# Optimization experiments

Measured on AMD Instinct MI355X. Metric: run time of the kernel, lower is better.

The kernel has to match this reference:

```python
import jax, jax.numpy as jnp
import numpy as np

B, S, D, H, DK, DFF = 4, 1024, 1024, 16, 64, 4096
EPS = 1e-5


def layer_norm(x, g, b):
    m = jnp.mean(x, axis=-1, keepdims=True)
    v = jnp.var(x, axis=-1, keepdims=True)
    return (x - m) * jax.lax.rsqrt(v + EPS) * g + b


def setup_inputs() -> dict:
    key = jax.random.key(0)
    ks = jax.random.split(key, 12)
    sc = 0.02
    return {
        "x":    jax.random.normal(ks[0], (B, S, D), jnp.float32),
        # per-head Q/K/V projections, stacked over heads: [H, D, DK]
        "Wq":   jax.random.normal(ks[1], (H, D, DK), jnp.float32) * sc,
        "bq":   jnp.zeros((H, DK), jnp.float32),
        "Wk":   jax.random.normal(ks[2], (H, D, DK), jnp.float32) * sc,
        "bk":   jnp.zeros((H, DK), jnp.float32),
        "Wv":   jax.random.normal(ks[3], (H, D, DK), jnp.float32) * sc,
        "bv":   jnp.zeros((H, DK), jnp.float32),
        # output projection: [H*DK, D]
        "Wo":   jax.random.normal(ks[4], (H * DK, D), jnp.float32) * sc,
        "bo":   jnp.zeros((D,), jnp.float32),
        # FFN
        "W1":   jax.random.normal(ks[5], (D, DFF), jnp.float32) * sc,
        "b1":   jnp.zeros((DFF,), jnp.float32),
        "W2":   jax.random.normal(ks[6], (DFF, D), jnp.float32) * sc,
        "b2":   jnp.zeros((D,), jnp.float32),
        # LayerNorms
        "g1":   jnp.ones((D,), jnp.float32),
        "be1":  jnp.zeros((D,), jnp.float32),
        "g2":   jnp.ones((D,), jnp.float32),
        "be2":  jnp.zeros((D,), jnp.float32),
    }


def reference(x, Wq, bq, Wk, bk, Wv, bv, Wo, bo, W1, b1, W2, b2, g1, be1, g2, be2):
    # batched multi-head attention (original loops per head; math identical)
    q = jnp.einsum("bsd,hdk->bhsk", x, Wq) + bq[None, :, None, :]
    k = jnp.einsum("bsd,hdk->bhsk", x, Wk) + bk[None, :, None, :]
    v = jnp.einsum("bsd,hdk->bhsk", x, Wv) + bv[None, :, None, :]
    scale = 1.0 / jnp.sqrt(jnp.asarray(DK, x.dtype))
    scores = jnp.einsum("bhsk,bhtk->bhst", q * scale, k)
    attn = jax.nn.softmax(scores, axis=-1)  # dropout = eval-mode identity
    o = jnp.einsum("bhst,bhtk->bhsk", attn, v)
    # torch.cat over heads along dim 2 -> [B, S, H*DK]
    o = jnp.transpose(o, (0, 2, 1, 3)).reshape(B, S, H * DK)
    att = o @ Wo + bo
    # post-attn: residual of LayerNorm(att)
    x = x + layer_norm(att, g1, be1)
    # FFN
    pos = jax.nn.relu(x @ W1 + b1) @ W2 + b2
    x = x + layer_norm(pos, g2, be2)
    return x
```

## Files before the change

kernel.cpp:

```cpp
#include <hip/hip_runtime.h>
#include <hip/hip_bf16.h>

typedef unsigned short u16;
typedef short bf16x8_t __attribute__((ext_vector_type(8)));
typedef float f32x4_t  __attribute__((ext_vector_type(4)));

__device__ __forceinline__ u16 f2bf(float f) {
    __hip_bfloat16 h = __float2bfloat16(f);
    union { __hip_bfloat16 b; u16 u; } cv; cv.b = h; return cv.u;
}

__device__ __forceinline__ void g2l16(const void* g, void* l) {
    __builtin_amdgcn_global_load_lds(
        (const __attribute__((address_space(1))) unsigned int*)g,
        (__attribute__((address_space(3))) unsigned int*)l, 16, 0, 0);
}

__global__ __launch_bounds__(256) void k_cast_bf16v(const float* __restrict__ in,
                                                    u16* __restrict__ out, int n4) {
    int i = blockIdx.x * 256 + threadIdx.x;
    if (i < n4) {
        float4 f = ((const float4*)in)[i];
        ushort4 o;
        o.x = f2bf(f.x); o.y = f2bf(f.y); o.z = f2bf(f.z); o.w = f2bf(f.w);
        ((ushort4*)out)[i] = o;
    }
}

__global__ __launch_bounds__(256)
void k_transpose3(const float* __restrict__ Wo, const float* __restrict__ W1,
                  const float* __restrict__ W2, u16* __restrict__ Wot,
                  u16* __restrict__ W1t, u16* __restrict__ W2t) {
    int id = blockIdx.x;
    const float* in; u16* out; int R, C, tx, ty;
    if (id < 256)       { in = Wo; out = Wot; R = 1024; C = 1024; tx = id & 15; ty = id >> 4; }
    else if (id < 1280) { id -= 256; in = W1; out = W1t; R = 1024; C = 4096; tx = id & 63; ty = id >> 6; }
    else                { id -= 1280; in = W2; out = W2t; R = 4096; C = 1024; tx = id & 15; ty = id >> 4; }
    __shared__ float t[64][65];
    int r0 = ty * 64, c0 = tx * 64;
    int lc = threadIdx.x & 63, lr = threadIdx.x >> 6;
#pragma unroll
    for (int p = 0; p < 16; ++p) {
        int rr = p * 4 + lr;
        t[rr][lc] = in[(size_t)(r0 + rr) * C + c0 + lc];
    }
    __syncthreads();
#pragma unroll
    for (int p = 0; p < 16; ++p) {
        int cc = p * 4 + lr;
        out[(size_t)(c0 + cc) * R + r0 + lc] = f2bf(t[lc][cc]);
    }
}

__global__ __launch_bounds__(256)
void k_qkvw_t(const float* __restrict__ Wq, const float* __restrict__ Wk,
              const float* __restrict__ Wv, u16* __restrict__ out) {
    const float* in = blockIdx.z == 0 ? Wq : (blockIdx.z == 1 ? Wk : Wv);
    in += (size_t)blockIdx.y * 65536;
    u16* o = out + ((size_t)blockIdx.z * 1024 + blockIdx.y * 64) * 1024;
    __shared__ float t[64][65];
    int d0 = blockIdx.x * 64;
    int lc = threadIdx.x & 63, lr = threadIdx.x >> 6;
#pragma unroll
    for (int p = 0; p < 16; ++p) {
        int rr = p * 4 + lr;
        t[rr][lc] = in[(size_t)(d0 + rr) * 64 + lc];
    }
    __syncthreads();
#pragma unroll
    for (int p = 0; p < 16; ++p) {
        int cc = p * 4 + lr;
        o[(size_t)cc * 1024 + d0 + lc] = f2bf(t[lc][cc]);
    }
}

__global__ __launch_bounds__(256)
void k_vt(const u16* __restrict__ V, u16* __restrict__ VT) {
    __shared__ u16 t[64 * 72];
    int bh = blockIdx.y, s0 = blockIdx.x * 64;
    const u16* Vp = V + (size_t)bh * 65536;
    u16* Tp = VT + (size_t)bh * 65536;
    int tid = threadIdx.x;
    int r = tid >> 3, c = (tid & 7) * 8;
    *(uint4*)&t[r * 72 + c]        = *(const uint4*)&Vp[(size_t)(s0 + r) * 64 + c];
    *(uint4*)&t[(r + 32) * 72 + c] = *(const uint4*)&Vp[(size_t)(s0 + r + 32) * 64 + c];
    __syncthreads();
    int d = tid >> 2, sl0 = (tid & 3) * 16;
    uint4 outv[2];
    u16* ov = (u16*)outv;
#pragma unroll
    for (int j = 0; j < 16; ++j) ov[j] = t[(sl0 + j) * 72 + d];
    *(uint4*)&Tp[(size_t)d * 1024 + s0 + sl0]     = outv[0];
    *(uint4*)&Tp[(size_t)d * 1024 + s0 + sl0 + 8] = outv[1];
}

template<int EPI>
__global__ __launch_bounds__(256)
void k_gemm_bt(const u16* __restrict__ A, const u16* __restrict__ Bt,
               const float* __restrict__ bias0, void* __restrict__ out,
               int M, int N, int K, int kchunk)
{
    __shared__ __align__(16) u16 As[2 * 128 * 32];
    __shared__ __align__(16) u16 Bs[2 * 128 * 32];
    int tid = threadIdx.x;
    int wave = tid >> 6, lane = tid & 63;
    int row0 = blockIdx.y * 128, col0 = blockIdx.x * 128;
    int z = blockIdx.z;
    int kbeg = z * kchunk;

    int lrow = lane >> 2, lcol = (lane & 3) * 8;
    const u16* pA0 = A  + (size_t)(row0 + wave * 16 + lrow) * K + kbeg + lcol;
    const u16* pA1 = pA0 + (size_t)64 * K;
    const u16* pB0 = Bt + (size_t)(col0 + wave * 16 + lrow) * K + kbeg + lcol;
    const u16* pB1 = pB0 + (size_t)64 * K;
    u16* lA0 = &As[wave * 512];
    u16* lA1 = &As[2048 + wave * 512];
    u16* lB0 = &Bs[wave * 512];
    u16* lB1 = &Bs[2048 + wave * 512];

    int wm = (wave >> 1) * 64, wn = (wave & 1) * 64;
    int quad = lane >> 4, l16 = lane & 15;

    f32x4_t acc[4][4];
#pragma unroll
    for (int i = 0; i < 4; i++)
#pragma unroll
        for (int j = 0; j < 4; j++) acc[i][j] = f32x4_t{0.f, 0.f, 0.f, 0.f};

    for (int kk = 0; kk < kchunk; kk += 64) {
        __syncthreads();
        g2l16(pA0, lA0);      g2l16(pA1, lA1);
        g2l16(pA0 + 32, lA0 + 4096); g2l16(pA1 + 32, lA1 + 4096);
        g2l16(pB0, lB0);      g2l16(pB1, lB1);
        g2l16(pB0 + 32, lB0 + 4096); g2l16(pB1 + 32, lB1 + 4096);
        pA0 += 64; pA1 += 64; pB0 += 64; pB1 += 64;
        __syncthreads();

#pragma unroll
        for (int s = 0; s < 2; ++s) {
            const u16* as = &As[s * 4096];
            const u16* bs = &Bs[s * 4096];
            bf16x8_t a[4], b[4];
#pragma unroll
            for (int i = 0; i < 4; ++i)
                a[i] = *(const bf16x8_t*)&as[(wm + i * 16 + l16) * 32 + quad * 8];
#pragma unroll
            for (int j = 0; j < 4; ++j)
                b[j] = *(const bf16x8_t*)&bs[(wn + j * 16 + l16) * 32 + quad * 8];
#pragma unroll
            for (int i = 0; i < 4; ++i)
#pragma unroll
                for (int j = 0; j < 4; ++j)
                    acc[i][j] = __builtin_amdgcn_mfma_f32_16x16x32_bf16(a[i], b[j], acc[i][j], 0, 0, 0);
        }
    }

#pragma unroll
    for (int i = 0; i < 4; ++i)
#pragma unroll
        for (int j = 0; j < 4; ++j)
#pragma unroll
            for (int r = 0; r < 4; ++r) {
                int row = row0 + wm + i * 16 + quad * 4 + r;
                int col = col0 + wn + j * 16 + l16;
                ((float*)out)[(size_t)z * M * N + (size_t)row * N + col] = acc[i][j][r];
            }
}

template<int EPI>
__global__ __launch_bounds__(512, 4)
void k_gemm_bt2(const u16* __restrict__ A, const u16* __restrict__ Bt,
                const float* __restrict__ bias0, const float* __restrict__ bias1,
                const float* __restrict__ bias2, void* __restrict__ out,
                int M, int N, int K)
{
    __shared__ __align__(16) u16 As[2 * 256 * 32];
    __shared__ __align__(16) u16 Bs[2 * 128 * 32];
    int tid = threadIdx.x;
    int wave = tid >> 6, lane = tid & 63;
    int row0 = blockIdx.y * 256, col0 = blockIdx.x * 128;

    int lrow = lane >> 2, lcol = (lane & 3) * 8;
    const u16* pA0 = A  + (size_t)(row0 + wave * 16 + lrow) * K + lcol;
    const u16* pA1 = pA0 + (size_t)128 * K;
    const u16* pB0 = Bt + (size_t)(col0 + wave * 16 + lrow) * K + lcol;
    u16* lA0 = &As[wave * 512];
    u16* lA1 = &As[4096 + wave * 512];
    u16* lB0 = &Bs[wave * 512];

    int wm = (wave >> 1) * 64, wn = (wave & 1) * 64;
    int quad = lane >> 4, l16 = lane & 15;

    f32x4_t acc[4][4];
#pragma unroll
    for (int i = 0; i < 4; i++)
#pragma unroll
        for (int j = 0; j < 4; j++) acc[i][j] = f32x4_t{0.f, 0.f, 0.f, 0.f};

    for (int kk = 0; kk < K; kk += 64) {
        __syncthreads();
        g2l16(pA0, lA0);           g2l16(pA1, lA1);
        g2l16(pA0 + 32, lA0 + 8192); g2l16(pA1 + 32, lA1 + 8192);
        g2l16(pB0, lB0);           g2l16(pB0 + 32, lB0 + 4096);
        pA0 += 64; pA1 += 64; pB0 += 64;
        __syncthreads();

#pragma unroll
        for (int s = 0; s < 2; ++s) {
            const u16* as = &As[s * 8192];
            const u16* bs = &Bs[s * 4096];
            bf16x8_t a[4], b[4];
#pragma unroll
            for (int i = 0; i < 4; ++i)
                a[i] = *(const bf16x8_t*)&as[(wm + i * 16 + l16) * 32 + quad * 8];
#pragma unroll
            for (int j = 0; j < 4; ++j)
                b[j] = *(const bf16x8_t*)&bs[(wn + j * 16 + l16) * 32 + quad * 8];
#pragma unroll
            for (int i = 0; i < 4; ++i)
#pragma unroll
                for (int j = 0; j < 4; ++j)
                    acc[i][j] = __builtin_amdgcn_mfma_f32_16x16x32_bf16(a[i], b[j], acc[i][j], 0, 0, 0);
        }
    }

#pragma unroll
    for (int i = 0; i < 4; ++i)
#pragma unroll
        for (int j = 0; j < 4; ++j)
#pragma unroll
            for (int r = 0; r < 4; ++r) {
                int row = row0 + wm + i * 16 + quad * 4 + r;
                int col = col0 + wn + j * 16 + l16;
                float v = acc[i][j][r];
                if (EPI == 1) {
                    ((u16*)out)[(size_t)row * N + col] = f2bf(fmaxf(v + bias0[col], 0.f));
                } else {
                    int proj = col >> 10, within = col & 1023;
                    const float* bp = proj == 0 ? bias0 : (proj == 1 ? bias1 : bias2);
                    v += bp[within];
                    if (proj == 0) v *= 0.18033688f;
                    int h = within >> 6, kq = within & 63;
                    int b_ = row >> 10, s_ = row & 1023;
                    size_t bh = (size_t)((b_ << 4) + h);
                    ((u16*)out)[(size_t)proj * 4194304 + bh * 65536 + (s_ << 6) + kq] = f2bf(v);
                }
            }
}

__global__ __launch_bounds__(512, 4)
void k_attn(const u16* __restrict__ Qg, const u16* __restrict__ Kg,
            const u16* __restrict__ VTg, u16* __restrict__ Og)
{
    __shared__ __align__(16) u16 Ks[64 * 64];
    __shared__ __align__(16) u16 Vs[64 * 64];
    __shared__ __align__(16) u16 Ps[128 * 64];

    int tid = threadIdx.x, wave = tid >> 6, lane = tid & 63;
    int quad = lane >> 4, l16 = lane & 15;
    int bh = blockIdx.y;
    int q0 = blockIdx.x * 128;
    int wrow = wave * 16;

    const u16* Qp  = Qg  + (size_t)bh * 65536;
    const u16* Kp  = Kg  + (size_t)bh * 65536;
    const u16* VTp = VTg + (size_t)bh * 65536;

    int arow_g = q0 + wrow + l16;
    bf16x8_t aq0 = *(const bf16x8_t*)&Qp[(size_t)arow_g * 64 + quad * 8];
    bf16x8_t aq1 = *(const bf16x8_t*)&Qp[(size_t)arow_g * 64 + 32 + quad * 8];

    int srow = tid >> 3, scb = tid & 7;
    uint4 kreg = *(const uint4*)&Kp[(size_t)srow * 64 + scb * 8];
    uint4 vreg = *(const uint4*)&VTp[(size_t)srow * 1024 + scb * 8];
    u16* kdst = &Ks[srow * 64 + ((scb ^ (srow & 7)) * 8)];
    u16* vdst = &Vs[srow * 64 + ((scb ^ (srow & 7)) * 8)];

    f32x4_t o[4], lsum;
#pragma unroll
    for (int nt = 0; nt < 4; ++nt) o[nt] = f32x4_t{0.f, 0.f, 0.f, 0.f};
    lsum = f32x4_t{0.f, 0.f, 0.f, 0.f};

    bf16x8_t ones;
#pragma unroll
    for (int j = 0; j < 8; ++j) ones[j] = (short)0x3F80;

    int a7 = l16 & 7;

    for (int kv0 = 0; kv0 < 1024; kv0 += 64) {
        __syncthreads();
        *(uint4*)kdst = kreg;
        *(uint4*)vdst = vreg;
        __syncthreads();
        if (kv0 < 960) {
            kreg = *(const uint4*)&Kp[(size_t)(kv0 + 64 + srow) * 64 + scb * 8];
            vreg = *(const uint4*)&VTp[(size_t)srow * 1024 + kv0 + 64 + scb * 8];
        }

        f32x4_t s[4];
#pragma unroll
        for (int nt = 0; nt < 4; ++nt) {
            int brow = nt * 16 + l16;
            bf16x8_t bk0 = *(const bf16x8_t*)&Ks[brow * 64 + ((quad ^ a7) * 8)];
            bf16x8_t bk1 = *(const bf16x8_t*)&Ks[brow * 64 + (((4 + quad) ^ a7) * 8)];
            s[nt] = __builtin_amdgcn_mfma_f32_16x16x32_bf16(aq0, bk0, f32x4_t{0.f,0.f,0.f,0.f}, 0, 0, 0);
            s[nt] = __builtin_amdgcn_mfma_f32_16x16x32_bf16(aq1, bk1, s[nt], 0, 0, 0);
        }

#pragma unroll
        for (int nt = 0; nt < 4; ++nt) {
            int pcb = nt * 2 + (l16 >> 3);
#pragma unroll
            for (int r = 0; r < 4; ++r) {
                float p = exp2f(s[nt][r]);
                int pr = wrow + quad * 4 + r;
                Ps[pr * 64 + ((pcb ^ (pr & 7)) * 8) + (l16 & 7)] = f2bf(p);
            }
        }

        int arow = wrow + l16;
        bf16x8_t ap0 = *(const bf16x8_t*)&Ps[arow * 64 + ((quad ^ a7) * 8)];
        bf16x8_t ap1 = *(const bf16x8_t*)&Ps[arow * 64 + (((4 + quad) ^ a7) * 8)];
#pragma unroll
        for (int nt = 0; nt < 4; ++nt) {
            int vrow = nt * 16 + l16;
            bf16x8_t bv0 = *(const bf16x8_t*)&Vs[vrow * 64 + ((quad ^ a7) * 8)];
            bf16x8_t bv1 = *(const bf16x8_t*)&Vs[vrow * 64 + (((4 + quad) ^ a7) * 8)];
            o[nt] = __builtin_amdgcn_mfma_f32_16x16x32_bf16(ap0, bv0, o[nt], 0, 0, 0);
            o[nt] = __builtin_amdgcn_mfma_f32_16x16x32_bf16(ap1, bv1, o[nt], 0, 0, 0);
        }
        lsum = __builtin_amdgcn_mfma_f32_16x16x32_bf16(ap0, ones, lsum, 0, 0, 0);
        lsum = __builtin_amdgcn_mfma_f32_16x16x32_bf16(ap1, ones, lsum, 0, 0, 0);
    }

    int b = bh >> 4, h = bh & 15;
    float invl[4];
#pragma unroll
    for (int r = 0; r < 4; ++r) invl[r] = 1.f / lsum[r];
#pragma unroll
    for (int nt = 0; nt < 4; ++nt)
#pragma unroll
        for (int r = 0; r < 4; ++r) {
            int srow2 = q0 + wrow + quad * 4 + r;
            Og[(size_t)(b * 1024 + srow2) * 1024 + (h << 6) + nt * 16 + l16] = f2bf(o[nt][r] * invl[r]);
        }
}

template<int MODE>
__global__ __launch_bounds__(256)
void k_ln2(const float* __restrict__ p0, const float* __restrict__ p1,
           const float* __restrict__ bias, const float* __restrict__ residf,
           const u16* __restrict__ residb, const float* __restrict__ g,
           const float* __restrict__ be, float* __restrict__ out,
           u16* __restrict__ outb)
{
    int row = blockIdx.x, tid = threadIdx.x;
    size_t base = (size_t)row * 1024;
    float xv[4]; float s = 0.f, sq = 0.f;
#pragma unroll
    for (int i = 0; i < 4; i++) {
        int c = tid + i * 256;
        xv[i] = p0[base + c] + p1[base + c] + bias[c];
        s += xv[i]; sq += xv[i] * xv[i];
    }
#pragma unroll
    for (int off = 32; off; off >>= 1) { s += __shfl_down(s, off); sq += __shfl_down(sq, off); }
    __shared__ float ss[4], ssq[4];
    int wv = tid >> 6;
    if ((tid & 63) == 0) { ss[wv] = s; ssq[wv] = sq; }
    __syncthreads();
    s  = ss[0] + ss[1] + ss[2] + ss[3];
    sq = ssq[0] + ssq[1] + ssq[2] + ssq[3];
    float mean = s * (1.f / 1024.f);
    float var  = sq * (1.f / 1024.f) - mean * mean;
    float rstd = rsqrtf(var + 1e-5f);
#pragma unroll
    for (int i = 0; i < 4; i++) {
        int c = tid + i * 256;
        float rv;
        if (MODE == 0) rv = residf[base + c];
        else {
            union { u16 u[2]; unsigned int w; float f; } cv;
            cv.w = (unsigned int)residb[base + c] << 16;
            rv = cv.f;
        }
        float y = rv + (xv[i] - mean) * rstd * g[c] + be[c];
        if (MODE == 0) outb[base + c] = f2bf(y);
        else           out[base + c] = y;
    }
}

extern "C" void kernel_launch(void* const* d_in, const int* in_sizes, int n_in,
                              void* d_out, int out_size, void* d_ws, size_t ws_size,
                              hipStream_t stream) {
    const float* x   = (const float*)d_in[0];
    const float* Wq  = (const float*)d_in[1];
    const float* bq  = (const float*)d_in[2];
    const float* Wk  = (const float*)d_in[3];
    const float* bk  = (const float*)d_in[4];
    const float* Wv  = (const float*)d_in[5];
    const float* bv  = (const float*)d_in[6];
    const float* Wo  = (const float*)d_in[7];
    const float* bo  = (const float*)d_in[8];
    const float* W1  = (const float*)d_in[9];
    const float* b1  = (const float*)d_in[10];
    const float* W2  = (const float*)d_in[11];
    const float* b2  = (const float*)d_in[12];
    const float* g1  = (const float*)d_in[13];
    const float* be1 = (const float*)d_in[14];
    const float* g2  = (const float*)d_in[15];
    const float* be2 = (const float*)d_in[16];
    float* out = (float*)d_out;

    char* w = (char*)d_ws;
    u16*   Xb    = (u16*)(w);
    u16*   VTb   = (u16*)(w);
    u16*   Wqkvt = (u16*)(w + 8388608);
    u16*   Wot   = (u16*)(w + 14680064);
    u16*   W1t   = (u16*)(w + 16777216);
    u16*   W2t   = (u16*)(w + 25165824);
    u16*   Qb    = (u16*)(w + 33554432);
    u16*   Kb    = (u16*)(w + 41943040);
    u16*   Vb    = (u16*)(w + 50331648);
    u16*   Oc    = (u16*)(w + 58720256);
    float* part  = (float*)(w + 67108864);
    u16*   x1b   = (u16*)(w + 117440512);
    u16*   hb    = (u16*)(w + 125829120);

    k_cast_bf16v<<<4096, 256, 0, stream>>>(x, Xb, 1048576);
    k_qkvw_t<<<dim3(16, 16, 3), 256, 0, stream>>>(Wq, Wk, Wv, Wqkvt);
    k_transpose3<<<2304, 256, 0, stream>>>(Wo, W1, W2, Wot, W1t, W2t);

    k_gemm_bt2<2><<<dim3(24, 16), 512, 0, stream>>>(Xb, Wqkvt, bq, bk, bv, Qb, 4096, 3072, 1024);

    k_vt<<<dim3(16, 64), 256, 0, stream>>>(Vb, VTb);

    k_attn<<<dim3(8, 64), 512, 0, stream>>>(Qb, Kb, VTb, Oc);

    k_gemm_bt<0><<<dim3(8, 32, 2), 256, 0, stream>>>(Oc, Wot, nullptr, part, 4096, 1024, 1024, 512);

    k_ln2<0><<<4096, 256, 0, stream>>>(part, part + 4194304, bo, x, nullptr, g1, be1, nullptr, x1b);

    k_gemm_bt2<1><<<dim3(32, 16), 512, 0, stream>>>(x1b, W1t, b1, nullptr, nullptr, hb, 4096, 4096, 1024);

    k_gemm_bt<0><<<dim3(8, 32, 2), 256, 0, stream>>>(hb, W2t, nullptr, part, 4096, 1024, 4096, 2048);

    k_ln2<1><<<4096, 256, 0, stream>>>(part, part + 4194304, b2, nullptr, x1b, g2, be2, out, nullptr);
}
```

Measured before the change: 335.7 us.

## Swizzle workgroup order for XCD locality and deepen split-K for FFN down-projection

Remaps the linear workgroup index in the split-K GEMM and in attention so that consecutive blocks dispatched to the same XCD share A/B tiles or the same head, aiming for better L2 reuse. The W2 GEMM now splits K four ways instead of two, putting 1024 workgroups in flight, and the LayerNorm kernel is templated over the number of partial sums it reduces. The GEMM also gets a minimum-occupancy launch bound of 4. In exchange, more fp32 partial traffic is written and read, and the partial buffer for the FFN reuses workspace that held Q/K/V.

```diff
diff --git a/kernel.cpp b/kernel.cpp
--- a/kernel.cpp
+++ b/kernel.cpp
@@ -95,7 +95,7 @@
 }
 
 template<int EPI>
-__global__ __launch_bounds__(256)
+__global__ __launch_bounds__(256, 4)
 void k_gemm_bt(const u16* __restrict__ A, const u16* __restrict__ Bt,
                const float* __restrict__ bias0, void* __restrict__ out,
                int M, int N, int K, int kchunk)
@@ -104,7 +104,13 @@
     __shared__ __align__(16) u16 Bs[2 * 128 * 32];
     int tid = threadIdx.x;
     int wave = tid >> 6, lane = tid & 63;
-    int row0 = blockIdx.y * 128, col0 = blockIdx.x * 128;
+
+    int nx = gridDim.x, nwg = nx * gridDim.y;
+    int f  = blockIdx.x + nx * blockIdx.y;
+    int f2 = (f & 7) * (nwg >> 3) + (f >> 3);
+    int bx = f2 % nx, by = f2 / nx;
+    int row0 = by * 128, col0 = bx * 128;
+
     int z = blockIdx.z;
     int kbeg = z * kchunk;
 
@@ -258,8 +264,11 @@
 
     int tid = threadIdx.x, wave = tid >> 6, lane = tid & 63;
     int quad = lane >> 4, l16 = lane & 15;
-    int bh = blockIdx.y;
-    int q0 = blockIdx.x * 128;
+
+    int f  = blockIdx.x + gridDim.x * blockIdx.y;
+    int f2 = (f & 7) * ((gridDim.x * gridDim.y) >> 3) + (f >> 3);
+    int bh = f2 >> 3;
+    int q0 = (f2 & 7) * 128;
     int wrow = wave * 16;
 
     const u16* Qp  = Qg  + (size_t)bh * 65536;
@@ -346,13 +355,12 @@
         }
 }
 
-template<int MODE>
+template<int MODE, int NP>
 __global__ __launch_bounds__(256)
-void k_ln2(const float* __restrict__ p0, const float* __restrict__ p1,
-           const float* __restrict__ bias, const float* __restrict__ residf,
-           const u16* __restrict__ residb, const float* __restrict__ g,
-           const float* __restrict__ be, float* __restrict__ out,
-           u16* __restrict__ outb)
+void k_ln2(const float* __restrict__ p, const float* __restrict__ bias,
+           const float* __restrict__ residf, const u16* __restrict__ residb,
+           const float* __restrict__ g, const float* __restrict__ be,
+           float* __restrict__ out, u16* __restrict__ outb)
 {
     int row = blockIdx.x, tid = threadIdx.x;
     size_t base = (size_t)row * 1024;
@@ -360,8 +368,11 @@
 #pragma unroll
     for (int i = 0; i < 4; i++) {
         int c = tid + i * 256;
-        xv[i] = p0[base + c] + p1[base + c] + bias[c];
-        s += xv[i]; sq += xv[i] * xv[i];
+        float t = bias[c];
+#pragma unroll
+        for (int z = 0; z < NP; ++z) t += p[(size_t)z * 4194304 + base + c];
+        xv[i] = t;
+        s += t; sq += t * t;
     }
 #pragma unroll
     for (int off = 32; off; off >>= 1) { s += __shfl_down(s, off); sq += __shfl_down(sq, off); }
@@ -423,7 +434,8 @@
     u16*   Kb    = (u16*)(w + 41943040);
     u16*   Vb    = (u16*)(w + 50331648);
     u16*   Oc    = (u16*)(w + 58720256);
-    float* part  = (float*)(w + 67108864);
+    float* part2 = (float*)(w + 67108864);
+    float* part4 = (float*)(w + 33554432);
     u16*   x1b   = (u16*)(w + 117440512);
     u16*   hb    = (u16*)(w + 125829120);
 
@@ -437,13 +449,13 @@
 
     k_attn<<<dim3(8, 64), 512, 0, stream>>>(Qb, Kb, VTb, Oc);
 
-    k_gemm_bt<0><<<dim3(8, 32, 2), 256, 0, stream>>>(Oc, Wot, nullptr, part, 4096, 1024, 1024, 512);
-
-    k_ln2<0><<<4096, 256, 0, stream>>>(part, part + 4194304, bo, x, nullptr, g1, be1, nullptr, x1b);
+    k_gemm_bt<0><<<dim3(8, 32, 2), 256, 0, stream>>>(Oc, Wot, nullptr, part2, 4096, 1024, 1024, 512);
+
+    k_ln2<0, 2><<<4096, 256, 0, stream>>>(part2, bo, x, nullptr, g1, be1, nullptr, x1b);
 
     k_gemm_bt2<1><<<dim3(32, 16), 512, 0, stream>>>(x1b, W1t, b1, nullptr, nullptr, hb, 4096, 4096, 1024);
 
-    k_gemm_bt<0><<<dim3(8, 32, 2), 256, 0, stream>>>(hb, W2t, nullptr, part, 4096, 1024, 4096, 2048);
-
-    k_ln2<1><<<4096, 256, 0, stream>>>(part, part + 4194304, b2, nullptr, x1b, g2, be2, out, nullptr);
-}
+    k_gemm_bt<0><<<dim3(8, 32, 4), 256, 0, stream>>>(hb, W2t, nullptr, part4, 4096, 1024, 4096, 1024);
+
+    k_ln2<1, 4><<<4096, 256, 0, stream>>>(part4, b2, nullptr, x1b, g2, be2, out, nullptr);
+}
```

After: 323.9 us. 3.5% less time.
